# Kernel optimization log

Hardware: AMD Instinct MI355X
Metric: run time of the kernel (lower is better)

## Reference

```python
import jax, jax.numpy as jnp
import numpy as np

D_MODEL = 1024
NHEAD = 16
DFF = 4096
EPS = 1e-5


def layer_norm(x, g, b, eps=EPS):
    mu = jnp.mean(x, axis=-1, keepdims=True)
    var = jnp.var(x, axis=-1, keepdims=True)
    return (x - mu) * jax.lax.rsqrt(var + eps) * g + b


def setup_inputs() -> dict:
    key = jax.random.key(0)
    ks = jax.random.split(key, 8)
    S, N, E = 1024, 8, D_MODEL
    s = 0.02
    return {
        "src": jax.random.normal(ks[0], (S, N, E), dtype=jnp.float32),
        "in_proj_w": jax.random.normal(ks[1], (3 * E, E), dtype=jnp.float32) * s,
        "in_proj_b": jnp.zeros((3 * E,), dtype=jnp.float32),
        "out_w": jax.random.normal(ks[2], (E, E), dtype=jnp.float32) * s,
        "out_b": jnp.zeros((E,), dtype=jnp.float32),
        "w1": jax.random.normal(ks[3], (DFF, E), dtype=jnp.float32) * s,
        "b1": jnp.zeros((DFF,), dtype=jnp.float32),
        "w2": jax.random.normal(ks[4], (E, DFF), dtype=jnp.float32) * s,
        "b2": jnp.zeros((E,), dtype=jnp.float32),
        "ln1_g": jnp.ones((E,), dtype=jnp.float32),
        "ln1_b": jnp.zeros((E,), dtype=jnp.float32),
        "ln2_g": jnp.ones((E,), dtype=jnp.float32),
        "ln2_b": jnp.zeros((E,), dtype=jnp.float32),
    }


def reference(src, in_proj_w, in_proj_b, out_w, out_b, w1, b1, w2, b2,
              ln1_g, ln1_b, ln2_g, ln2_b):
    S, N, E = src.shape
    H = NHEAD
    D = E // H
    scale = 1.0 / jnp.sqrt(jnp.asarray(D, src.dtype))

    # fused QKV projection (PyTorch in_proj): [S,N,3E]
    qkv = src @ in_proj_w.T + in_proj_b
    q, k, v = jnp.split(qkv, 3, axis=-1)
    # [S,N,E] -> [N,H,S,D]
    def to_heads(t):
        return t.reshape(S, N, H, D).transpose(1, 2, 0, 3)
    q, k, v = to_heads(q), to_heads(k), to_heads(v)

    # explicit QK^T / softmax / AV (need_weights=True path)
    scores = jnp.einsum('nhsd,nhtd->nhst', q * scale, k)  # [N,H,S,S]
    attn = jax.nn.softmax(scores, axis=-1)
    ctx = jnp.einsum('nhst,nhtd->nhsd', attn, v)          # [N,H,S,D]
    ctx = ctx.transpose(2, 0, 1, 3).reshape(S, N, E)
    attn_out = ctx @ out_w.T + out_b

    # avg over heads (PyTorch default average_attn_weights=True): [N,S,S]
    attn_weights = jnp.mean(attn, axis=1)

    # post-norm residual structure (norm_first=False), dropout=0 (eval)
    x = layer_norm(src + attn_out, ln1_g, ln1_b)
    ff = jax.nn.relu(x @ w1.T + b1) @ w2.T + b2
    x = layer_norm(x + ff, ln2_g, ln2_b)
    return x, attn_weights
```

## Files before the change

### kernel.cpp

```cpp
#include <hip/hip_runtime.h>

typedef __attribute__((ext_vector_type(4))) float f32x4;
typedef __attribute__((ext_vector_type(8))) short short8;
typedef __attribute__((ext_vector_type(4))) unsigned short u16x4;

#define MFMA(a,b,c) __builtin_amdgcn_mfma_f32_16x16x32_bf16(a,b,c,0,0,0)

__device__ __forceinline__ unsigned short f2bf(float x){
    union { float f; unsigned int u; } c; c.f = x;
    unsigned int u = c.u;
    unsigned int r = (u + 0x7fffu + ((u >> 16) & 1u)) >> 16;
    return (unsigned short)r;
}
__device__ __forceinline__ float bf2f(unsigned short h){
    union { unsigned int u; float f; } c; c.u = ((unsigned int)h) << 16;
    return c.f;
}

__device__ __forceinline__ void load16_lds(const unsigned short* g, unsigned short* l){
    __builtin_amdgcn_global_load_lds(
        (const __attribute__((address_space(1))) unsigned int*)g,
        (__attribute__((address_space(3))) unsigned int*)l, 16, 0, 0);
}

#define SWZ_IDX(row, col, stride) \
    ((row)*(stride) + (((((col) >> 3) ^ ((row) & 7)) << 3) | ((col) & 7)))

__global__ __launch_bounds__(256) void cast_f32_bf16(const float* __restrict__ in,
                                                     unsigned short* __restrict__ out, int n4){
    int i = blockIdx.x * 256 + threadIdx.x;
    if (i < n4){
        const float4* in4 = (const float4*)in;
        float4 v = in4[i];
        u16x4 o;
        o[0] = f2bf(v.x); o[1] = f2bf(v.y); o[2] = f2bf(v.z); o[3] = f2bf(v.w);
        ((u16x4*)out)[i] = o;
    }
}

template<int OUT_BF16, int RELU>
__global__ __launch_bounds__(256) void gemm_bt(const unsigned short* __restrict__ A,
                                               const unsigned short* __restrict__ W,
                                               const float* __restrict__ bias,
                                               void* __restrict__ Cout,
                                               int M, int N, int K)
{
    __shared__ unsigned short As[128*32];
    __shared__ unsigned short Bs[128*32];
    const int tid  = threadIdx.x;
    const int wave = tid >> 6, lane = tid & 63;
    const int bm = blockIdx.x, bn = blockIdx.y;
    const int wr = wave >> 1, wc = wave & 1;
    const int lr = lane & 15, lg = lane >> 4;

    f32x4 acc[4][4] = {};

    const size_t arow0 = (size_t)bm * 128;
    const size_t brow0 = (size_t)bn * 128;

    for (int k0 = 0; k0 < K; k0 += 32){
        __syncthreads();
        #pragma unroll
        for (int i = 0; i < 2; ++i){
            int c = i*256 + wave*64 + lane;
            int row = c >> 2, cc = c & 3;
            load16_lds(A + (arow0 + row)*K + k0 + cc*8, As + (size_t)(i*256 + wave*64)*8);
            load16_lds(W + (brow0 + row)*K + k0 + cc*8, Bs + (size_t)(i*256 + wave*64)*8);
        }
        __syncthreads();
        short8 af[4], bfr[4];
        #pragma unroll
        for (int mi = 0; mi < 4; ++mi)
            af[mi] = *(const short8*)(As + (wr*64 + mi*16 + lr)*32 + lg*8);
        #pragma unroll
        for (int ni = 0; ni < 4; ++ni)
            bfr[ni] = *(const short8*)(Bs + (wc*64 + ni*16 + lr)*32 + lg*8);
        #pragma unroll
        for (int mi = 0; mi < 4; ++mi)
            #pragma unroll
            for (int ni = 0; ni < 4; ++ni)
                acc[mi][ni] = MFMA(af[mi], bfr[ni], acc[mi][ni]);
    }

    #pragma unroll
    for (int ni = 0; ni < 4; ++ni){
        int col = bn*128 + wc*64 + ni*16 + lr;
        float bv = bias ? bias[col] : 0.0f;
        #pragma unroll
        for (int mi = 0; mi < 4; ++mi){
            int row0 = bm*128 + wr*64 + mi*16 + lg*4;
            #pragma unroll
            for (int j = 0; j < 4; ++j){
                float v = acc[mi][ni][j] + bv;
                if (RELU) v = v > 0.0f ? v : 0.0f;
                if (OUT_BF16) ((unsigned short*)Cout)[(size_t)(row0+j)*N + col] = f2bf(v);
                else          ((float*)Cout)[(size_t)(row0+j)*N + col] = v;
            }
        }
    }
}

template<int OUT_BF16, int RELU>
__global__ __launch_bounds__(512) void gemm256(const unsigned short* __restrict__ A,
                                               const unsigned short* __restrict__ W,
                                               const float* __restrict__ bias,
                                               void* __restrict__ Cout,
                                               int M, int N, int K)
{
    __shared__ unsigned short Asw[2][256*64];
    __shared__ unsigned short Bsw[2][256*64];
    const int tid  = threadIdx.x;
    const int wave = tid >> 6, lane = tid & 63;
    const int wr = wave >> 2, wc = wave & 3;
    const int lr = lane & 15, lg = lane >> 4;
    const int bm = blockIdx.x, bn = blockIdx.y;

    f32x4 acc[8][4] = {};

    const unsigned short* Ab = A + (size_t)bm*256*K;
    const unsigned short* Wb = W + (size_t)bn*256*K;

    auto stage = [&](int buf, int k0){
        #pragma unroll
        for (int i = 0; i < 4; ++i){
            int c = i*512 + tid;
            int row = c >> 3, sl = (c & 7) ^ (row & 7);
            load16_lds(Ab + (size_t)row*K + k0 + sl*8, &Asw[buf][0] + (size_t)c*8);
        }
        #pragma unroll
        for (int i = 0; i < 4; ++i){
            int c = i*512 + tid;
            int row = c >> 3, sl = (c & 7) ^ (row & 7);
            load16_lds(Wb + (size_t)row*K + k0 + sl*8, &Bsw[buf][0] + (size_t)c*8);
        }
    };

    stage(0, 0);
    const int NT = K >> 6;
    for (int t = 0; t < NT; ++t){
        const int cur = t & 1;
        if (t + 1 < NT){
            stage(cur ^ 1, (t+1) << 6);
            asm volatile("s_waitcnt vmcnt(8)" ::: "memory");
        } else {
            asm volatile("s_waitcnt vmcnt(0)" ::: "memory");
        }
        __builtin_amdgcn_s_barrier();
        asm volatile("" ::: "memory");
        const unsigned short* Al = &Asw[cur][0];
        const unsigned short* Bl = &Bsw[cur][0];
        #pragma unroll
        for (int kk = 0; kk < 2; ++kk){
            short8 af[8], bf[4];
            #pragma unroll
            for (int mi = 0; mi < 8; ++mi)
                af[mi] = *(const short8*)(Al + SWZ_IDX(wr*128 + mi*16 + lr, kk*32 + lg*8, 64));
            #pragma unroll
            for (int ni = 0; ni < 4; ++ni)
                bf[ni] = *(const short8*)(Bl + SWZ_IDX(wc*64 + ni*16 + lr, kk*32 + lg*8, 64));
            __builtin_amdgcn_s_setprio(1);
            #pragma unroll
            for (int mi = 0; mi < 8; ++mi)
                #pragma unroll
                for (int ni = 0; ni < 4; ++ni)
                    acc[mi][ni] = MFMA(af[mi], bf[ni], acc[mi][ni]);
            __builtin_amdgcn_s_setprio(0);
        }
        asm volatile("" ::: "memory");
        __builtin_amdgcn_s_barrier();
    }

    #pragma unroll
    for (int ni = 0; ni < 4; ++ni){
        int col = bn*256 + wc*64 + ni*16 + lr;
        float bv = bias ? bias[col] : 0.0f;
        #pragma unroll
        for (int mi = 0; mi < 8; ++mi){
            int row0 = bm*256 + wr*128 + mi*16 + lg*4;
            #pragma unroll
            for (int j = 0; j < 4; ++j){
                float v = acc[mi][ni][j] + bv;
                if (RELU) v = v > 0.0f ? v : 0.0f;
                if (OUT_BF16) ((unsigned short*)Cout)[(size_t)(row0+j)*N + col] = f2bf(v);
                else          ((float*)Cout)[(size_t)(row0+j)*N + col] = v;
            }
        }
    }
}

__global__ __launch_bounds__(256) void transpose_v(const unsigned short* __restrict__ qkv,
                                                   unsigned short* __restrict__ vt)
{
    __shared__ unsigned short tile[64][80];
    const int tt = blockIdx.x, h = blockIdx.y, n = blockIdx.z;
    const int tid = threadIdx.x;
    #pragma unroll
    for (int i = 0; i < 2; ++i){
        int c = i*256 + tid;
        int row = c >> 3, cc = c & 7;
        short8 v = *(const short8*)(qkv + ((size_t)(tt*64+row)*8 + n)*3072 + 2048 + h*64 + cc*8);
        *(short8*)&tile[row][cc*8] = v;
    }
    __syncthreads();
    #pragma unroll
    for (int i = 0; i < 2; ++i){
        int c = i*256 + tid;
        int drow = c >> 3, cc = c & 7;
        short8 o;
        #pragma unroll
        for (int j = 0; j < 8; ++j) o[j] = tile[cc*8+j][drow];
        *(short8*)(vt + ((size_t)(n*16+h)*64 + drow)*1024 + tt*64 + cc*8) = o;
    }
}

__global__ __launch_bounds__(256) void attn_fused(const unsigned short* __restrict__ qkv,
                                                  const unsigned short* __restrict__ vt,
                                                  float2* __restrict__ stats,
                                                  unsigned short* __restrict__ ctx)
{
    __shared__ unsigned short qs[32*64];
    __shared__ unsigned short kt[64*64];
    __shared__ unsigned short vtile[64*64];
    __shared__ unsigned short pt[32*64];
    __shared__ float wl[4][32];
    __shared__ float rowinv[32];
    const int qb = blockIdx.x, h = blockIdx.y, n = blockIdx.z;
    const int tid = threadIdx.x;
    const int wave = tid >> 6, lane = tid & 63;
    const int lr = lane & 15, lg = lane >> 4;
    const int s0 = qb * 32;
    const float scale = 0.125f;

    {
        int row = tid >> 3, cc = tid & 7;
        *(short8*)(qs + SWZ_IDX(row, cc*8, 64)) =
            *(const short8*)(qkv + ((size_t)(s0+row)*8 + n)*3072 + h*64 + cc*8);
    }

    float lsum[2][4] = {};
    f32x4 av[2] = {};

    for (int tt = 0; tt < 16; ++tt){
        __syncthreads();
        #pragma unroll
        for (int i = 0; i < 2; ++i){
            int c = i*256 + wave*64 + lane;
            int row = c >> 3, sl = (c & 7) ^ (row & 7);
            load16_lds(qkv + ((size_t)(tt*64+row)*8 + n)*3072 + 1024 + h*64 + sl*8,
                       kt + (size_t)(i*256 + wave*64)*8);
            load16_lds(vt + ((size_t)(n*16+h)*64 + row)*1024 + tt*64 + sl*8,
                       vtile + (size_t)(i*256 + wave*64)*8);
        }
        __syncthreads();

        f32x4 acc[2] = {};
        #pragma unroll
        for (int kk = 0; kk < 2; ++kk){
            short8 b  = *(const short8*)(kt + SWZ_IDX(wave*16 + lr, kk*32 + lg*8, 64));
            short8 a0 = *(const short8*)(qs + SWZ_IDX(lr,          kk*32 + lg*8, 64));
            short8 a1 = *(const short8*)(qs + SWZ_IDX(16 + lr,     kk*32 + lg*8, 64));
            acc[0] = MFMA(a0, b, acc[0]);
            acc[1] = MFMA(a1, b, acc[1]);
        }
        #pragma unroll
        for (int mi = 0; mi < 2; ++mi)
            #pragma unroll
            for (int j = 0; j < 4; ++j){
                float p = __expf(fminf(acc[mi][j] * scale, 80.0f));
                lsum[mi][j] += p;
                pt[SWZ_IDX(mi*16 + lg*4 + j, wave*16 + lr, 64)] = f2bf(p);
            }
        __syncthreads();

        #pragma unroll
        for (int kk = 0; kk < 2; ++kk){
            short8 b  = *(const short8*)(vtile + SWZ_IDX(wave*16 + lr, kk*32 + lg*8, 64));
            short8 a0 = *(const short8*)(pt + SWZ_IDX(lr,      kk*32 + lg*8, 64));
            short8 a1 = *(const short8*)(pt + SWZ_IDX(16 + lr, kk*32 + lg*8, 64));
            av[0] = MFMA(a0, b, av[0]);
            av[1] = MFMA(a1, b, av[1]);
        }
    }

    #pragma unroll
    for (int mi = 0; mi < 2; ++mi)
        #pragma unroll
        for (int j = 0; j < 4; ++j){
            float v = lsum[mi][j];
            v += __shfl_xor(v, 1);
            v += __shfl_xor(v, 2);
            v += __shfl_xor(v, 4);
            v += __shfl_xor(v, 8);
            if (lr == 0) wl[wave][mi*16 + lg*4 + j] = v;
        }
    __syncthreads();
    if (tid < 32){
        float l = wl[0][tid] + wl[1][tid] + wl[2][tid] + wl[3][tid];
        float inv = 1.0f / l;
        rowinv[tid] = inv;
        stats[((size_t)(n*16+h)*1024) + s0 + tid] = make_float2(0.0f, inv * 0.0625f);
    }
    __syncthreads();

    #pragma unroll
    for (int mi = 0; mi < 2; ++mi)
        #pragma unroll
        for (int j = 0; j < 4; ++j){
            int lrow = mi*16 + lg*4 + j;
            int srow = s0 + lrow;
            int d = wave*16 + lr;
            ctx[((size_t)srow*8 + n)*1024 + h*64 + d] = f2bf(av[mi][j] * rowinv[lrow]);
        }
}

__global__ __launch_bounds__(256) void attn_mean(const unsigned short* __restrict__ qkv,
                                                 const float2* __restrict__ stats,
                                                 float* __restrict__ attw)
{
    __shared__ unsigned short qs[16*1024];
    __shared__ unsigned short kv[2][4][16*128];
    __shared__ float2 smL[16][16];
    const int qb = blockIdx.x, n = blockIdx.y;
    const int tid = threadIdx.x;
    const int wave = tid >> 6, lane = tid & 63;
    const int lr = lane & 15, lg = lane >> 4;
    const int s0 = qb * 16;
    const float scale = 0.125f;

    {
        int head = tid >> 4, row = tid & 15;
        smL[head][row] = stats[((size_t)(n*16+head)*1024) + s0 + row];
    }
    #pragma unroll
    for (int i = 0; i < 8; ++i){
        int c = i*256 + tid;
        int row = c >> 7, cc = c & 127;
        *(short8*)(qs + SWZ_IDX(row, cc*8, 1024)) =
            *(const short8*)(qkv + ((size_t)(s0+row)*8 + n)*3072 + cc*8);
    }

    unsigned short* kvw = &kv[0][wave][0];
    const int KVBUF = 4*16*128;

    auto stage = [&](int buf, int tt, int g){
        #pragma unroll
        for (int i = 0; i < 4; ++i){
            int c2 = i*64 + lane;
            int rw = c2 >> 4;
            int sd = c2 & 15;
            int sl = sd ^ (rw & 7);
            int trow = tt*64 + wave*16 + rw;
            load16_lds(qkv + ((size_t)trow*8 + n)*3072 + 1024 + g*128 + sl*8,
                       kvw + buf*KVBUF + i*512);
        }
    };

    __syncthreads();
    stage(0, 0, 0);

    float* obase = attw + (size_t)n*1024*1024;
    int r = 0;
    for (int tt = 0; tt < 16; ++tt){
        f32x4 racc = {0.0f, 0.0f, 0.0f, 0.0f};
        for (int g = 0; g < 8; ++g, ++r){
            int nr = r + 1;
            if (nr < 128) stage(nr & 1, nr >> 3, nr & 7);
            if (r < 127) asm volatile("s_waitcnt vmcnt(4)" ::: "memory");
            else         asm volatile("s_waitcnt vmcnt(0)" ::: "memory");
            const unsigned short* kb = kvw + (r & 1)*KVBUF;
            #pragma unroll
            for (int hh = 0; hh < 2; ++hh){
                f32x4 acc = {0.0f, 0.0f, 0.0f, 0.0f};
                #pragma unroll
                for (int kk = 0; kk < 2; ++kk){
                    short8 b = *(const short8*)(kb + SWZ_IDX(lr, hh*64 + kk*32 + lg*8, 128));
                    short8 a = *(const short8*)(qs + SWZ_IDX(lr, g*128 + hh*64 + kk*32 + lg*8, 1024));
                    acc = MFMA(a, b, acc);
                }
                #pragma unroll
                for (int j = 0; j < 4; ++j){
                    float2 mc = smL[g*2 + hh][lg*4 + j];
                    racc[j] += __expf(fminf(acc[j]*scale, 80.0f) - mc.x) * mc.y;
                }
            }
        }
        #pragma unroll
        for (int j = 0; j < 4; ++j)
            obase[(size_t)(s0 + lg*4 + j)*1024 + tt*64 + wave*16 + lr] = racc[j];
    }
}

__global__ __launch_bounds__(256) void add_ln(const float* __restrict__ a,
                                              const float* __restrict__ b,
                                              const float* __restrict__ g,
                                              const float* __restrict__ be,
                                              float* __restrict__ out32,
                                              unsigned short* __restrict__ outbf)
{
    __shared__ float red[8];
    const int row = blockIdx.x;
    const int tid = threadIdx.x;
    const int wave = tid >> 6, lane = tid & 63;
    float4 va = ((const float4*)(a + (size_t)row*1024))[tid];
    float4 vb = ((const float4*)(b + (size_t)row*1024))[tid];
    float x0 = va.x + vb.x, x1 = va.y + vb.y, x2 = va.z + vb.z, x3 = va.w + vb.w;
    float s  = x0 + x1 + x2 + x3;
    float sq = x0*x0 + x1*x1 + x2*x2 + x3*x3;
    #pragma unroll
    for (int off = 1; off < 64; off <<= 1){
        s  += __shfl_xor(s,  off);
        sq += __shfl_xor(sq, off);
    }
    if (lane == 0){ red[wave] = s; red[4+wave] = sq; }
    __syncthreads();
    s  = red[0] + red[1] + red[2] + red[3];
    sq = red[4] + red[5] + red[6] + red[7];
    float mean = s * (1.0f/1024.0f);
    float var  = sq * (1.0f/1024.0f) - mean*mean;
    float rstd = rsqrtf(var + 1e-5f);
    int c = tid * 4;
    float4 vg = ((const float4*)(g  + c))[0];
    float4 vbeta = ((const float4*)(be + c))[0];
    float y0 = (x0-mean)*rstd*vg.x + vbeta.x;
    float y1 = (x1-mean)*rstd*vg.y + vbeta.y;
    float y2 = (x2-mean)*rstd*vg.z + vbeta.z;
    float y3 = (x3-mean)*rstd*vg.w + vbeta.w;
    float4 o; o.x=y0; o.y=y1; o.z=y2; o.w=y3;
    ((float4*)(out32 + (size_t)row*1024))[tid] = o;
    if (outbf){
        u16x4 ob; ob[0]=f2bf(y0); ob[1]=f2bf(y1); ob[2]=f2bf(y2); ob[3]=f2bf(y3);
        ((u16x4*)(outbf + (size_t)row*1024))[tid] = ob;
    }
}

extern "C" void kernel_launch(void* const* d_in, const int* in_sizes, int n_in,
                              void* d_out, int out_size, void* d_ws, size_t ws_size,
                              hipStream_t stream)
{
    (void)in_sizes; (void)n_in; (void)out_size; (void)ws_size;
    const float* src  = (const float*)d_in[0];
    const float* wqkv = (const float*)d_in[1];
    const float* bqkv = (const float*)d_in[2];
    const float* wout = (const float*)d_in[3];
    const float* bout = (const float*)d_in[4];
    const float* w1   = (const float*)d_in[5];
    const float* b1   = (const float*)d_in[6];
    const float* w2   = (const float*)d_in[7];
    const float* b2   = (const float*)d_in[8];
    const float* g1   = (const float*)d_in[9];
    const float* be1  = (const float*)d_in[10];
    const float* g2   = (const float*)d_in[11];
    const float* be2  = (const float*)d_in[12];

    char* ws = (char*)d_ws;
    const size_t MB = 1ull << 20;
    unsigned short* wqkv_bf = (unsigned short*)(ws + 0*MB);
    unsigned short* wout_bf = (unsigned short*)(ws + 6*MB);
    unsigned short* w1_bf   = (unsigned short*)(ws + 8*MB);
    unsigned short* w2_bf   = (unsigned short*)(ws + 16*MB);
    unsigned short* src_bf  = (unsigned short*)(ws + 24*MB);
    unsigned short* x1_bf   = (unsigned short*)(ws + 24*MB);
    unsigned short* qkv_bf  = (unsigned short*)(ws + 40*MB);
    unsigned short* vt_bf   = (unsigned short*)(ws + 88*MB);
    unsigned short* ff1_bf  = (unsigned short*)(ws + 40*MB);
    unsigned short* ctx_bf  = (unsigned short*)(ws + 104*MB);
    float* attn_out = (float*)(ws + 120*MB);
    float* ff2_f32  = (float*)(ws + 120*MB);
    float* x1_f32   = (float*)(ws + 152*MB);
    float2* stats   = (float2*)(ws + 184*MB);

    float* x_out    = (float*)d_out;
    float* attw_out = (float*)d_out + (size_t)8192*1024;

    auto cast = [&](const float* in, unsigned short* out, int nelem){
        int n4 = nelem / 4;
        hipLaunchKernelGGL(cast_f32_bf16, dim3((n4 + 255)/256), dim3(256), 0, stream, in, out, n4);
    };
    cast(wqkv, wqkv_bf, 3072*1024);
    cast(wout, wout_bf, 1024*1024);
    cast(w1,   w1_bf,   4096*1024);
    cast(w2,   w2_bf,   1024*4096);
    cast(src,  src_bf,  8192*1024);

    hipLaunchKernelGGL((gemm256<1,0>), dim3(32,12), dim3(512), 0, stream,
                       src_bf, wqkv_bf, bqkv, (void*)qkv_bf, 8192, 3072, 1024);
    hipLaunchKernelGGL(transpose_v, dim3(16,16,8), dim3(256), 0, stream, qkv_bf, vt_bf);
    hipLaunchKernelGGL(attn_fused, dim3(32,16,8), dim3(256), 0, stream,
                       qkv_bf, vt_bf, stats, ctx_bf);
    hipLaunchKernelGGL(attn_mean, dim3(64,8), dim3(256), 0, stream,
                       qkv_bf, stats, attw_out);
    hipLaunchKernelGGL((gemm_bt<0,0>), dim3(64,8), dim3(256), 0, stream,
                       ctx_bf, wout_bf, bout, (void*)attn_out, 8192, 1024, 1024);
    hipLaunchKernelGGL(add_ln, dim3(8192), dim3(256), 0, stream,
                       src, attn_out, g1, be1, x1_f32, x1_bf);
    hipLaunchKernelGGL((gemm256<1,1>), dim3(32,16), dim3(512), 0, stream,
                       x1_bf, w1_bf, b1, (void*)ff1_bf, 8192, 4096, 1024);
    hipLaunchKernelGGL((gemm_bt<0,0>), dim3(64,8), dim3(256), 0, stream,
                       ff1_bf, w2_bf, b2, (void*)ff2_f32, 8192, 1024, 4096);
    hipLaunchKernelGGL(add_ln, dim3(8192), dim3(256), 0, stream,
                       x1_f32, ff2_f32, g2, be2, x_out, nullptr);
}
```

Baseline: 559.2 us.

## Replace simple 128x128 GEMM with double-buffered swizzled 256x128 kernel for N=1024 GEMMs

Adds a gemm256x128 kernel that uses 512 threads, double-buffered LDS with XOR swizzling, async global-to-LDS prefetch of the next K tile, and MFMA priority hints. It replaces the old single-buffered 128x128 gemm_bt in the out-projection and FFN down-projection GEMMs. The goal is to overlap memory loads with MFMA work and avoid LDS bank conflicts. Only 256 blocks are launched, which may underfill the GPU's compute units and costs more LDS per block.

```diff
diff --git a/kernel.cpp b/kernel.cpp
--- a/kernel.cpp
+++ b/kernel.cpp
@@ -39,68 +39,6 @@
 }
 
 template<int OUT_BF16, int RELU>
-__global__ __launch_bounds__(256) void gemm_bt(const unsigned short* __restrict__ A,
-                                               const unsigned short* __restrict__ W,
-                                               const float* __restrict__ bias,
-                                               void* __restrict__ Cout,
-                                               int M, int N, int K)
-{
-    __shared__ unsigned short As[128*32];
-    __shared__ unsigned short Bs[128*32];
-    const int tid  = threadIdx.x;
-    const int wave = tid >> 6, lane = tid & 63;
-    const int bm = blockIdx.x, bn = blockIdx.y;
-    const int wr = wave >> 1, wc = wave & 1;
-    const int lr = lane & 15, lg = lane >> 4;
-
-    f32x4 acc[4][4] = {};
-
-    const size_t arow0 = (size_t)bm * 128;
-    const size_t brow0 = (size_t)bn * 128;
-
-    for (int k0 = 0; k0 < K; k0 += 32){
-        __syncthreads();
-        #pragma unroll
-        for (int i = 0; i < 2; ++i){
-            int c = i*256 + wave*64 + lane;
-            int row = c >> 2, cc = c & 3;
-            load16_lds(A + (arow0 + row)*K + k0 + cc*8, As + (size_t)(i*256 + wave*64)*8);
-            load16_lds(W + (brow0 + row)*K + k0 + cc*8, Bs + (size_t)(i*256 + wave*64)*8);
-        }
-        __syncthreads();
-        short8 af[4], bfr[4];
-        #pragma unroll
-        for (int mi = 0; mi < 4; ++mi)
-            af[mi] = *(const short8*)(As + (wr*64 + mi*16 + lr)*32 + lg*8);
-        #pragma unroll
-        for (int ni = 0; ni < 4; ++ni)
-            bfr[ni] = *(const short8*)(Bs + (wc*64 + ni*16 + lr)*32 + lg*8);
-        #pragma unroll
-        for (int mi = 0; mi < 4; ++mi)
-            #pragma unroll
-            for (int ni = 0; ni < 4; ++ni)
-                acc[mi][ni] = MFMA(af[mi], bfr[ni], acc[mi][ni]);
-    }
-
-    #pragma unroll
-    for (int ni = 0; ni < 4; ++ni){
-        int col = bn*128 + wc*64 + ni*16 + lr;
-        float bv = bias ? bias[col] : 0.0f;
-        #pragma unroll
-        for (int mi = 0; mi < 4; ++mi){
-            int row0 = bm*128 + wr*64 + mi*16 + lg*4;
-            #pragma unroll
-            for (int j = 0; j < 4; ++j){
-                float v = acc[mi][ni][j] + bv;
-                if (RELU) v = v > 0.0f ? v : 0.0f;
-                if (OUT_BF16) ((unsigned short*)Cout)[(size_t)(row0+j)*N + col] = f2bf(v);
-                else          ((float*)Cout)[(size_t)(row0+j)*N + col] = v;
-            }
-        }
-    }
-}
-
-template<int OUT_BF16, int RELU>
 __global__ __launch_bounds__(512) void gemm256(const unsigned short* __restrict__ A,
                                                const unsigned short* __restrict__ W,
                                                const float* __restrict__ bias,
@@ -177,6 +115,94 @@
         #pragma unroll
         for (int mi = 0; mi < 8; ++mi){
             int row0 = bm*256 + wr*128 + mi*16 + lg*4;
+            #pragma unroll
+            for (int j = 0; j < 4; ++j){
+                float v = acc[mi][ni][j] + bv;
+                if (RELU) v = v > 0.0f ? v : 0.0f;
+                if (OUT_BF16) ((unsigned short*)Cout)[(size_t)(row0+j)*N + col] = f2bf(v);
+                else          ((float*)Cout)[(size_t)(row0+j)*N + col] = v;
+            }
+        }
+    }
+}
+
+template<int OUT_BF16, int RELU>
+__global__ __launch_bounds__(512) void gemm256x128(const unsigned short* __restrict__ A,
+                                                   const unsigned short* __restrict__ W,
+                                                   const float* __restrict__ bias,
+                                                   void* __restrict__ Cout,
+                                                   int M, int N, int K)
+{
+    __shared__ unsigned short Asw[2][256*64];
+    __shared__ unsigned short Bsw[2][128*64];
+    const int tid  = threadIdx.x;
+    const int wave = tid >> 6, lane = tid & 63;
+    const int wr = wave >> 1, wc = wave & 1;
+    const int lr = lane & 15, lg = lane >> 4;
+    const int bm = blockIdx.x, bn = blockIdx.y;
+
+    f32x4 acc[4][4] = {};
+
+    const unsigned short* Ab = A + (size_t)bm*256*K;
+    const unsigned short* Wb = W + (size_t)bn*128*K;
+
+    auto stage = [&](int buf, int k0){
+        #pragma unroll
+        for (int i = 0; i < 4; ++i){
+            int c = i*512 + tid;
+            int row = c >> 3, sl = (c & 7) ^ (row & 7);
+            load16_lds(Ab + (size_t)row*K + k0 + sl*8, &Asw[buf][0] + (size_t)c*8);
+        }
+        #pragma unroll
+        for (int i = 0; i < 2; ++i){
+            int c = i*512 + tid;
+            int row = c >> 3, sl = (c & 7) ^ (row & 7);
+            load16_lds(Wb + (size_t)row*K + k0 + sl*8, &Bsw[buf][0] + (size_t)c*8);
+        }
+    };
+
+    stage(0, 0);
+    const int NT = K >> 6;
+    for (int t = 0; t < NT; ++t){
+        const int cur = t & 1;
+        if (t + 1 < NT){
+            stage(cur ^ 1, (t+1) << 6);
+            asm volatile("s_waitcnt vmcnt(6)" ::: "memory");
+        } else {
+            asm volatile("s_waitcnt vmcnt(0)" ::: "memory");
+        }
+        __builtin_amdgcn_s_barrier();
+        asm volatile("" ::: "memory");
+        const unsigned short* Al = &Asw[cur][0];
+        const unsigned short* Bl = &Bsw[cur][0];
+        #pragma unroll
+        for (int kk = 0; kk < 2; ++kk){
+            short8 af[4], bf[4];
+            #pragma unroll
+            for (int mi = 0; mi < 4; ++mi)
+                af[mi] = *(const short8*)(Al + SWZ_IDX(wr*64 + mi*16 + lr, kk*32 + lg*8, 64));
+            #pragma unroll
+            for (int ni = 0; ni < 4; ++ni)
+                bf[ni] = *(const short8*)(Bl + SWZ_IDX(wc*64 + ni*16 + lr, kk*32 + lg*8, 64));
+            __builtin_amdgcn_s_setprio(1);
+            #pragma unroll
+            for (int mi = 0; mi < 4; ++mi)
+                #pragma unroll
+                for (int ni = 0; ni < 4; ++ni)
+                    acc[mi][ni] = MFMA(af[mi], bf[ni], acc[mi][ni]);
+            __builtin_amdgcn_s_setprio(0);
+        }
+        asm volatile("" ::: "memory");
+        __builtin_amdgcn_s_barrier();
+    }
+
+    #pragma unroll
+    for (int ni = 0; ni < 4; ++ni){
+        int col = bn*128 + wc*64 + ni*16 + lr;
+        float bv = bias ? bias[col] : 0.0f;
+        #pragma unroll
+        for (int mi = 0; mi < 4; ++mi){
+            int row0 = bm*256 + wr*64 + mi*16 + lg*4;
             #pragma unroll
             for (int j = 0; j < 4; ++j){
                 float v = acc[mi][ni][j] + bv;
@@ -489,13 +515,13 @@
                        qkv_bf, vt_bf, stats, ctx_bf);
     hipLaunchKernelGGL(attn_mean, dim3(64,8), dim3(256), 0, stream,
                        qkv_bf, stats, attw_out);
-    hipLaunchKernelGGL((gemm_bt<0,0>), dim3(64,8), dim3(256), 0, stream,
+    hipLaunchKernelGGL((gemm256x128<0,0>), dim3(32,8), dim3(512), 0, stream,
                        ctx_bf, wout_bf, bout, (void*)attn_out, 8192, 1024, 1024);
     hipLaunchKernelGGL(add_ln, dim3(8192), dim3(256), 0, stream,
                        src, attn_out, g1, be1, x1_f32, x1_bf);
     hipLaunchKernelGGL((gemm256<1,1>), dim3(32,16), dim3(512), 0, stream,
                        x1_bf, w1_bf, b1, (void*)ff1_bf, 8192, 4096, 1024);
-    hipLaunchKernelGGL((gemm_bt<0,0>), dim3(64,8), dim3(256), 0, stream,
+    hipLaunchKernelGGL((gemm256x128<0,0>), dim3(32,8), dim3(512), 0, stream,
                        ff1_bf, w2_bf, b2, (void*)ff2_f32, 8192, 1024, 4096);
     hipLaunchKernelGGL(add_ln, dim3(8192), dim3(256), 0, stream,
                        x1_f32, ff2_f32, g2, be2, x_out, nullptr);
```

After: 545.5 us. 1.03x faster.
